# Kernel optimization log

Measured on AMD Instinct MI355X. Metric: run time of the kernel, lower is better.

## Reference

```python
import jax, jax.numpy as jnp
import numpy as np

N_NODES = 100000
N_EDGES = 1600000
NODE_F = 8   # augmented node features
EDGE_F = 2   # augmented edge features
GLOB_F = 1
HID = 16
L = 3        # message passing steps

EDGE_IN = GLOB_F + EDGE_F + 2 * NODE_F   # 19
NODE_IN = GLOB_F + EDGE_F + NODE_F       # 11
GLOB_IN = EDGE_F + NODE_F + GLOB_F       # 11


def setup_inputs() -> dict:
    key = jax.random.key(0)
    ks = jax.random.split(key, 20)
    inp = {
        "x": jax.random.normal(ks[0], (N_NODES, NODE_F), dtype=jnp.float32),
        "edge_index": jax.random.randint(ks[1], (2, N_EDGES), 0, N_NODES, dtype=jnp.int32),
        "edge_attr": jax.random.normal(ks[2], (N_EDGES, EDGE_F), dtype=jnp.float32),
        "g": jax.random.normal(ks[3], (1, GLOB_F), dtype=jnp.float32),
    }
    s = 0.1
    inp["edge_W1"] = jax.random.normal(ks[4], (L, EDGE_IN, HID), dtype=jnp.float32) * s
    inp["edge_b1"] = jnp.zeros((L, HID), dtype=jnp.float32)
    inp["edge_W2"] = jax.random.normal(ks[5], (L, HID, EDGE_F), dtype=jnp.float32) * s
    inp["edge_b2"] = jnp.zeros((L, EDGE_F), dtype=jnp.float32)
    inp["node_W1"] = jax.random.normal(ks[6], (L, NODE_IN, HID), dtype=jnp.float32) * s
    inp["node_b1"] = jnp.zeros((L, HID), dtype=jnp.float32)
    inp["node_W2"] = jax.random.normal(ks[7], (L, HID, NODE_F), dtype=jnp.float32) * s
    inp["node_b2"] = jnp.zeros((L, NODE_F), dtype=jnp.float32)
    inp["glob_W1"] = jax.random.normal(ks[8], (L, GLOB_IN, HID), dtype=jnp.float32) * s
    inp["glob_b1"] = jnp.zeros((L, HID), dtype=jnp.float32)
    inp["glob_W2"] = jax.random.normal(ks[9], (L, HID, GLOB_F), dtype=jnp.float32) * s
    inp["glob_b2"] = jnp.zeros((L, GLOB_F), dtype=jnp.float32)
    return inp


def _mlp(h, W1, b1, W2, b2):
    # two-layer MLP with ReLU after first layer only (activate_final=False, no layer_norm)
    return jnp.maximum(h @ W1 + b1, 0.0) @ W2 + b2


def reference(x, edge_index, edge_attr, g,
              edge_W1, edge_b1, edge_W2, edge_b2,
              node_W1, node_b1, node_W2, node_b2,
              glob_W1, glob_b1, glob_W2, glob_b2):
    row, col = edge_index[0], edge_index[1]
    n = x.shape[0]
    for l in range(L):
        g_e = jnp.broadcast_to(g, (row.shape[0], GLOB_F))
        # edge block: gather node features along edges, concat, MLP -> [E, EDGE_F]
        e_in = jnp.concatenate([g_e, x[row], x[col], edge_attr], axis=1)
        edge_emb = _mlp(e_in, edge_W1[l], edge_b1[l], edge_W2[l], edge_b2[l])
        # sum-aggregate edge embeddings to source nodes
        agg = jax.ops.segment_sum(edge_emb, row, num_segments=n)
        g_n = jnp.broadcast_to(g, (n, GLOB_F))
        node_emb = _mlp(jnp.concatenate([g_n, x, agg], axis=1),
                        node_W1[l], node_b1[l], node_W2[l], node_b2[l])
        # global block on mean-aggregated edge/node embeddings
        edge_gl = jnp.mean(edge_emb, axis=0, keepdims=True)
        node_gl = jnp.mean(node_emb, axis=0, keepdims=True)
        g = _mlp(jnp.concatenate([node_gl, edge_gl, g], axis=1),
                 glob_W1[l], glob_b1[l], glob_W2[l], glob_b2[l])
        x, edge_attr = node_emb, edge_emb
    return x  # final node embeddings [N, NODE_F]
```

## Files before the change

kernel.cpp:

```cpp
#include <hip/hip_runtime.h>

#define NN 100000
#define NE 1600000
#define CH 4096
#define NCHUNK ((NE + CH - 1) / CH)
#define NBUCK ((NN + 255) / 256)
#define SUB 4

__device__ __forceinline__ float wave_red(float v) {
#pragma unroll
    for (int off = 32; off > 0; off >>= 1) v += __shfl_down(v, off, 64);
    return v;
}

__global__ __launch_bounds__(256) void hist_kernel(
    const int* __restrict__ ei, int* __restrict__ hist)
{
    __shared__ int h[NBUCK];
    int t = threadIdx.x, c = blockIdx.x;
    for (int b = t; b < NBUCK; b += 256) h[b] = 0;
    __syncthreads();
    int base = c * CH;
    for (int i = t; i < CH; i += 256) {
        int e = base + i;
        if (e < NE) atomicAdd(&h[ei[e] >> 8], 1);
    }
    __syncthreads();
    for (int b = t; b < NBUCK; b += 256) hist[c * NBUCK + b] = h[b];
}

__global__ __launch_bounds__(512) void bscan_kernel(
    const int* __restrict__ hist, int* __restrict__ baseT, int* __restrict__ colTotal)
{
    __shared__ int buf[2][512];
    int b = blockIdx.x, t = threadIdx.x;
    int v = (t < NCHUNK) ? hist[t * NBUCK + b] : 0;
    buf[0][t] = v;
    __syncthreads();
    int src = 0;
    for (int d = 1; d < 512; d <<= 1) {
        int nv = buf[src][t] + ((t >= d) ? buf[src][t - d] : 0);
        buf[src ^ 1][t] = nv;
        src ^= 1;
        __syncthreads();
    }
    if (t < NCHUNK) baseT[b * NCHUNK + t] = buf[src][t] - v;
    if (t == NCHUNK - 1) colTotal[b] = buf[src][t];
}

__global__ __launch_bounds__(512) void boff_kernel(
    const int* __restrict__ colTotal, int* __restrict__ b_off)
{
    __shared__ int buf[2][512];
    int t = threadIdx.x;
    int v = (t < NBUCK) ? colTotal[t] : 0;
    buf[0][t] = v;
    __syncthreads();
    int src = 0;
    for (int d = 1; d < 512; d <<= 1) {
        int nv = buf[src][t] + ((t >= d) ? buf[src][t - d] : 0);
        buf[src ^ 1][t] = nv;
        src ^= 1;
        __syncthreads();
    }
    if (t < NBUCK) b_off[t] = buf[src][t] - v;
    if (t == NBUCK - 1) b_off[NBUCK] = buf[src][t];
}

__global__ __launch_bounds__(256) void fillb_kernel(
    const int* __restrict__ ei, const float* __restrict__ eattr,
    const int* __restrict__ baseT, const int* __restrict__ b_off,
    float4* __restrict__ rec)
{
    __shared__ int sslot[NBUCK];
    int t = threadIdx.x, c = blockIdx.x;
    for (int b = t; b < NBUCK; b += 256)
        sslot[b] = b_off[b] + baseT[b * NCHUNK + c];
    __syncthreads();
    int base = c * CH;
    for (int i = t; i < CH; i += 256) {
        int e = base + i;
        if (e < NE) {
            int row = ei[e];
            int slot = atomicAdd(&sslot[row >> 8], 1);
            float2 ea = reinterpret_cast<const float2*>(eattr)[e];
            float4 v;
            v.x = __int_as_float(row);
            v.y = __int_as_float(ei[NE + e]);
            v.z = ea.x; v.w = ea.y;
            rec[slot] = v;
        }
    }
}

template <bool WRITE_EMB, bool NEED_SUM>
__global__ __launch_bounds__(256, 1) void edge_kernel(
    float4* __restrict__ rec, const int* __restrict__ b_off,
    const float* __restrict__ gptr,
    const float* __restrict__ eW1, const float* __restrict__ eB1,
    const float* __restrict__ eW2, const float* __restrict__ eB2,
    const float* __restrict__ xin,
    float2* __restrict__ pagg, float* __restrict__ sums)
{
    __shared__ float sPr[256][20];
    __shared__ float sagg[256][2];
    __shared__ float redE[4][2];
    int tid = threadIdx.x;
    int b = blockIdx.x >> 2, s = blockIdx.x & 3;
    int n0 = b << 8;
    sagg[tid][0] = 0.f; sagg[tid][1] = 0.f;

    float gval = gptr[0];
    int nrow = n0 + tid;
    if (nrow < NN) {
        const float4* xi = reinterpret_cast<const float4*>(xin + (size_t)nrow * 8);
        float4 a0 = xi[0], a1 = xi[1];
        float xv[8] = {a0.x, a0.y, a0.z, a0.w, a1.x, a1.y, a1.z, a1.w};
        float pr[16];
#pragma unroll
        for (int q = 0; q < 16; q++) pr[q] = 0.f;
#pragma unroll
        for (int k = 0; k < 8; k++) {
            float v = xv[k];
#pragma unroll
            for (int q = 0; q < 16; q++) pr[q] += v * eW1[(1 + k) * 16 + q];
        }
        float4* pw = reinterpret_cast<float4*>(&sPr[tid][0]);
#pragma unroll
        for (int t4 = 0; t4 < 4; t4++)
            pw[t4] = make_float4(pr[4*t4], pr[4*t4+1], pr[4*t4+2], pr[4*t4+3]);
    }
    __syncthreads();

    float cw[128], aw[32], ow[32], gterm[16];
    {
        const float4* W4 = reinterpret_cast<const float4*>(eW1 + 9 * 16);
#pragma unroll
        for (int i = 0; i < 32; i++) {
            float4 w = W4[i];
            cw[4*i] = w.x; cw[4*i+1] = w.y; cw[4*i+2] = w.z; cw[4*i+3] = w.w;
        }
        const float4* A4 = reinterpret_cast<const float4*>(eW1 + 17 * 16);
#pragma unroll
        for (int i = 0; i < 8; i++) {
            float4 w = A4[i];
            aw[4*i] = w.x; aw[4*i+1] = w.y; aw[4*i+2] = w.z; aw[4*i+3] = w.w;
        }
        const float4* O4 = reinterpret_cast<const float4*>(eW2);
#pragma unroll
        for (int i = 0; i < 8; i++) {
            float4 w = O4[i];
            ow[4*i] = w.x; ow[4*i+1] = w.y; ow[4*i+2] = w.z; ow[4*i+3] = w.w;
        }
#pragma unroll
        for (int q = 0; q < 16; q++) gterm[q] = eB1[q] + gval * eW1[q];
    }
    float b20 = eB2[0], b21 = eB2[1];

    int e0b = b_off[b], e1b = b_off[b + 1];
    int qlen = (e1b - e0b + SUB - 1) / SUB;
    int es = e0b + s * qlen;
    int ee = min(e1b, es + qlen);

    float t0 = 0.f, t1 = 0.f;
    for (int e = es + tid; e < ee; e += 256) {
        float4 r = rec[e];
        int li  = __float_as_int(r.x) - n0;
        int col = __float_as_int(r.y);
        const float4* xc4 = reinterpret_cast<const float4*>(xin + (size_t)col * 8);
        float4 c0 = xc4[0], c1 = xc4[1];
        const float4* pr4 = reinterpret_cast<const float4*>(&sPr[li][0]);
        float4 p0 = pr4[0], p1 = pr4[1], p2 = pr4[2], p3 = pr4[3];
        float h[16];
        h[0]  = gterm[0]  + p0.x; h[1]  = gterm[1]  + p0.y;
        h[2]  = gterm[2]  + p0.z; h[3]  = gterm[3]  + p0.w;
        h[4]  = gterm[4]  + p1.x; h[5]  = gterm[5]  + p1.y;
        h[6]  = gterm[6]  + p1.z; h[7]  = gterm[7]  + p1.w;
        h[8]  = gterm[8]  + p2.x; h[9]  = gterm[9]  + p2.y;
        h[10] = gterm[10] + p2.z; h[11] = gterm[11] + p2.w;
        h[12] = gterm[12] + p3.x; h[13] = gterm[13] + p3.y;
        h[14] = gterm[14] + p3.z; h[15] = gterm[15] + p3.w;
        float xc[8] = {c0.x, c0.y, c0.z, c0.w, c1.x, c1.y, c1.z, c1.w};
#pragma unroll
        for (int k = 0; k < 8; k++) {
            float v = xc[k];
#pragma unroll
            for (int q = 0; q < 16; q++) h[q] += v * cw[k * 16 + q];
        }
#pragma unroll
        for (int q = 0; q < 16; q++) h[q] += r.z * aw[q] + r.w * aw[16 + q];
        float s0 = b20, s1 = b21;
#pragma unroll
        for (int q = 0; q < 16; q++) {
            float rr = fmaxf(h[q], 0.f);
            s0 += rr * ow[2 * q];
            s1 += rr * ow[2 * q + 1];
        }
        if (WRITE_EMB) rec[e] = make_float4(r.x, r.y, s0, s1);
        atomicAdd(&sagg[li][0], s0);
        atomicAdd(&sagg[li][1], s1);
        t0 += s0; t1 += s1;
    }

    if (NEED_SUM) {
        float r0 = wave_red(t0), r1 = wave_red(t1);
        int wave = tid >> 6, lane = tid & 63;
        if (lane == 0) { redE[wave][0] = r0; redE[wave][1] = r1; }
    }
    __syncthreads();
    pagg[((size_t)s * NBUCK + b) * 256 + tid] =
        make_float2(sagg[tid][0], sagg[tid][1]);
    if (NEED_SUM && tid == 0) {
        atomicAdd(&sums[0], redE[0][0] + redE[1][0] + redE[2][0] + redE[3][0]);
        atomicAdd(&sums[1], redE[0][1] + redE[1][1] + redE[2][1] + redE[3][1]);
    }
}

template <bool NEED_SUM>
__global__ __launch_bounds__(256) void node_kernel(
    const float* __restrict__ xin, const float2* __restrict__ pagg,
    const float* __restrict__ gptr,
    const float* __restrict__ nW1, const float* __restrict__ nB1,
    const float* __restrict__ nW2, const float* __restrict__ nB2,
    float* __restrict__ xout, float* __restrict__ sums)
{
    __shared__ float redN[4][8];
    int tid = threadIdx.x, b = blockIdx.x;
    int n = b * 256 + tid;
    float out[8];
#pragma unroll
    for (int m = 0; m < 8; m++) out[m] = 0.f;

    if (n < NN) {
        float ag0 = 0.f, ag1 = 0.f;
#pragma unroll
        for (int s = 0; s < SUB; s++) {
            float2 p = pagg[((size_t)s * NBUCK + b) * 256 + tid];
            ag0 += p.x; ag1 += p.y;
        }
        float gval = gptr[0];
        float in[11];
        in[0] = gval;
        const float4* xi = reinterpret_cast<const float4*>(xin + (size_t)n * 8);
        float4 a0 = xi[0], a1 = xi[1];
        in[1] = a0.x; in[2] = a0.y; in[3] = a0.z; in[4] = a0.w;
        in[5] = a1.x; in[6] = a1.y; in[7] = a1.z; in[8] = a1.w;
        in[9] = ag0; in[10] = ag1;

        float h[16];
#pragma unroll
        for (int q = 0; q < 16; q++) h[q] = nB1[q];
#pragma unroll
        for (int k = 0; k < 11; k++) {
            float v = in[k];
#pragma unroll
            for (int q = 0; q < 16; q++) h[q] += v * nW1[k * 16 + q];
        }
#pragma unroll
        for (int m = 0; m < 8; m++) out[m] = nB2[m];
#pragma unroll
        for (int q = 0; q < 16; q++) {
            float hq = fmaxf(h[q], 0.f);
#pragma unroll
            for (int m = 0; m < 8; m++) out[m] += hq * nW2[q * 8 + m];
        }
        float4* xo = reinterpret_cast<float4*>(xout + (size_t)n * 8);
        xo[0] = make_float4(out[0], out[1], out[2], out[3]);
        xo[1] = make_float4(out[4], out[5], out[6], out[7]);
    }
    if (NEED_SUM) {
        float r[8];
#pragma unroll
        for (int m = 0; m < 8; m++) r[m] = wave_red(out[m]);
        int wave = tid >> 6, lane = tid & 63;
        if (lane == 0) {
#pragma unroll
            for (int m = 0; m < 8; m++) redN[wave][m] = r[m];
        }
        __syncthreads();
        if (tid == 0) {
#pragma unroll
            for (int m = 0; m < 8; m++) {
                float s = redN[0][m] + redN[1][m] + redN[2][m] + redN[3][m];
                atomicAdd(&sums[2 + m], s);
            }
        }
    }
}

__global__ void glob_kernel(const float* __restrict__ sums,
                            const float* __restrict__ gold,
                            const float* __restrict__ W1, const float* __restrict__ B1,
                            const float* __restrict__ W2, const float* __restrict__ B2,
                            float* __restrict__ gnew)
{
    if (threadIdx.x == 0 && blockIdx.x == 0) {
        float in[11];
#pragma unroll
        for (int j = 0; j < 8; j++) in[j] = sums[2 + j] * (1.0f / NN);
        in[8] = sums[0] * (1.0f / NE);
        in[9] = sums[1] * (1.0f / NE);
        in[10] = gold[0];
        float acc = B2[0];
#pragma unroll
        for (int j = 0; j < 16; j++) {
            float h = B1[j];
#pragma unroll
            for (int k = 0; k < 11; k++) h += in[k] * W1[k * 16 + j];
            acc += fmaxf(h, 0.f) * W2[j];
        }
        gnew[0] = acc;
    }
}

extern "C" void kernel_launch(void* const* d_in, const int* in_sizes, int n_in,
                              void* d_out, int out_size, void* d_ws, size_t ws_size,
                              hipStream_t stream) {
    const float* x     = (const float*)d_in[0];
    const int*   ei    = (const int*)d_in[1];
    const float* eattr = (const float*)d_in[2];
    const float* g     = (const float*)d_in[3];
    const float* eW1 = (const float*)d_in[4];
    const float* eB1 = (const float*)d_in[5];
    const float* eW2 = (const float*)d_in[6];
    const float* eB2 = (const float*)d_in[7];
    const float* nW1 = (const float*)d_in[8];
    const float* nB1 = (const float*)d_in[9];
    const float* nW2 = (const float*)d_in[10];
    const float* nB2 = (const float*)d_in[11];
    const float* gW1 = (const float*)d_in[12];
    const float* gB1 = (const float*)d_in[13];
    const float* gW2 = (const float*)d_in[14];
    const float* gB2 = (const float*)d_in[15];
    float* out = (float*)d_out;

    char* ws = (char*)d_ws;
    float*  xb0   = (float*)(ws);
    float*  xb1   = (float*)(ws + 3200000);
    int*    b_off = (int*)  (ws + 6400000);
    float*  sums  = (float*)(ws + 6401600);
    float*  g1    = (float*)(ws + 6401728);
    float*  g2    = g1 + 1;
    float4* rec   = (float4*)(ws + 6401792);
    float2* pagg  = (float2*)(ws + 32001792);
    int*    hist     = (int*)xb1;
    int*    baseT    = (int*)((char*)xb1 + 611584);
    int*    colTotal = (int*)((char*)xb1 + 1223168);

    dim3 blk(256);
    dim3 cgrid(NCHUNK);
    dim3 bgrid(NBUCK);
    dim3 egrid(NBUCK * SUB);

    hipMemsetAsync(sums, 0, 128, stream);
    hist_kernel<<<cgrid, blk, 0, stream>>>(ei, hist);
    bscan_kernel<<<bgrid, 512, 0, stream>>>(hist, baseT, colTotal);
    boff_kernel<<<1, 512, 0, stream>>>(colTotal, b_off);
    fillb_kernel<<<cgrid, blk, 0, stream>>>(ei, eattr, baseT, b_off, rec);

    edge_kernel<true, true><<<egrid, blk, 0, stream>>>(
        rec, b_off, g, eW1, eB1, eW2, eB2, x, pagg, sums);
    node_kernel<true><<<bgrid, blk, 0, stream>>>(
        x, pagg, g, nW1, nB1, nW2, nB2, xb0, sums);
    glob_kernel<<<1, 64, 0, stream>>>(sums, g, gW1, gB1, gW2, gB2, g1);

    edge_kernel<true, true><<<egrid, blk, 0, stream>>>(
        rec, b_off, g1, eW1 + 304, eB1 + 16, eW2 + 32, eB2 + 2, xb0, pagg, sums + 16);
    node_kernel<true><<<bgrid, blk, 0, stream>>>(
        xb0, pagg, g1, nW1 + 176, nB1 + 16, nW2 + 128, nB2 + 8, xb1, sums + 16);
    glob_kernel<<<1, 64, 0, stream>>>(sums + 16, g1, gW1 + 176, gB1 + 16, gW2 + 16, gB2 + 1, g2);

    edge_kernel<false, false><<<egrid, blk, 0, stream>>>(
        rec, b_off, g2, eW1 + 608, eB1 + 32, eW2 + 64, eB2 + 4, xb1, pagg, sums);
    node_kernel<false><<<bgrid, blk, 0, stream>>>(
        xb1, pagg, g2, nW1 + 352, nB1 + 32, nW2 + 256, nB2 + 16, out, sums);
}
```

Measured before the change: 388.0 us.

## Fuse node MLP into edge kernel via last-block-done counter

The node update now runs inside the edge kernel: each of the four sub-blocks per node bucket bumps a per-bucket atomic counter, and the last one to finish reads the partial aggregates and computes the node MLP. This removes three node kernel launches and their inter-kernel gaps. It also folds the bias and global term into the per-node precompute, writes only the two embedding floats back to the record, and pins the weight arrays in registers with empty asm. The cost is threadfences, extra counter memory that must be zeroed each call, and higher register pressure in the edge kernel.

Measured after the change: 1.134 ms. +192.4%, slower.

```diff
diff --git a/kernel.cpp b/kernel.cpp
--- a/kernel.cpp
+++ b/kernel.cpp
@@ -100,11 +100,16 @@
     const float* __restrict__ eW1, const float* __restrict__ eB1,
     const float* __restrict__ eW2, const float* __restrict__ eB2,
     const float* __restrict__ xin,
-    float2* __restrict__ pagg, float* __restrict__ sums)
+    const float* __restrict__ nW1, const float* __restrict__ nB1,
+    const float* __restrict__ nW2, const float* __restrict__ nB2,
+    float2* __restrict__ pagg, int* __restrict__ cnt,
+    float* __restrict__ xout, float* __restrict__ sums)
 {
     __shared__ float sPr[256][20];
     __shared__ float sagg[256][2];
     __shared__ float redE[4][2];
+    __shared__ float redN[4][8];
+    __shared__ int   isLast;
     int tid = threadIdx.x;
     int b = blockIdx.x >> 2, s = blockIdx.x & 3;
     int n0 = b << 8;
@@ -118,7 +123,7 @@
         float xv[8] = {a0.x, a0.y, a0.z, a0.w, a1.x, a1.y, a1.z, a1.w};
         float pr[16];
 #pragma unroll
-        for (int q = 0; q < 16; q++) pr[q] = 0.f;
+        for (int q = 0; q < 16; q++) pr[q] = eB1[q] + gval * eW1[q];
 #pragma unroll
         for (int k = 0; k < 8; k++) {
             float v = xv[k];
@@ -132,7 +137,7 @@
     }
     __syncthreads();
 
-    float cw[128], aw[32], ow[32], gterm[16];
+    float cw[128], aw[32], ow[32];
     {
         const float4* W4 = reinterpret_cast<const float4*>(eW1 + 9 * 16);
 #pragma unroll
@@ -152,9 +157,13 @@
             float4 w = O4[i];
             ow[4*i] = w.x; ow[4*i+1] = w.y; ow[4*i+2] = w.z; ow[4*i+3] = w.w;
         }
-#pragma unroll
-        for (int q = 0; q < 16; q++) gterm[q] = eB1[q] + gval * eW1[q];
-    }
+    }
+#pragma unroll
+    for (int i = 0; i < 128; i++) asm volatile("" : "+v"(cw[i]));
+#pragma unroll
+    for (int i = 0; i < 32; i++)  asm volatile("" : "+v"(aw[i]));
+#pragma unroll
+    for (int i = 0; i < 32; i++)  asm volatile("" : "+v"(ow[i]));
     float b20 = eB2[0], b21 = eB2[1];
 
     int e0b = b_off[b], e1b = b_off[b + 1];
@@ -172,14 +181,10 @@
         const float4* pr4 = reinterpret_cast<const float4*>(&sPr[li][0]);
         float4 p0 = pr4[0], p1 = pr4[1], p2 = pr4[2], p3 = pr4[3];
         float h[16];
-        h[0]  = gterm[0]  + p0.x; h[1]  = gterm[1]  + p0.y;
-        h[2]  = gterm[2]  + p0.z; h[3]  = gterm[3]  + p0.w;
-        h[4]  = gterm[4]  + p1.x; h[5]  = gterm[5]  + p1.y;
-        h[6]  = gterm[6]  + p1.z; h[7]  = gterm[7]  + p1.w;
-        h[8]  = gterm[8]  + p2.x; h[9]  = gterm[9]  + p2.y;
-        h[10] = gterm[10] + p2.z; h[11] = gterm[11] + p2.w;
-        h[12] = gterm[12] + p3.x; h[13] = gterm[13] + p3.y;
-        h[14] = gterm[14] + p3.z; h[15] = gterm[15] + p3.w;
+        h[0]  = p0.x; h[1]  = p0.y; h[2]  = p0.z; h[3]  = p0.w;
+        h[4]  = p1.x; h[5]  = p1.y; h[6]  = p1.z; h[7]  = p1.w;
+        h[8]  = p2.x; h[9]  = p2.y; h[10] = p2.z; h[11] = p2.w;
+        h[12] = p3.x; h[13] = p3.y; h[14] = p3.z; h[15] = p3.w;
         float xc[8] = {c0.x, c0.y, c0.z, c0.w, c1.x, c1.y, c1.z, c1.w};
 #pragma unroll
         for (int k = 0; k < 8; k++) {
@@ -196,7 +201,8 @@
             s0 += rr * ow[2 * q];
             s1 += rr * ow[2 * q + 1];
         }
-        if (WRITE_EMB) rec[e] = make_float4(r.x, r.y, s0, s1);
+        if (WRITE_EMB)
+            reinterpret_cast<float2*>(rec)[2 * e + 1] = make_float2(s0, s1);
         atomicAdd(&sagg[li][0], s0);
         atomicAdd(&sagg[li][1], s1);
         t0 += s0; t1 += s1;
@@ -214,31 +220,23 @@
         atomicAdd(&sums[0], redE[0][0] + redE[1][0] + redE[2][0] + redE[3][0]);
         atomicAdd(&sums[1], redE[0][1] + redE[1][1] + redE[2][1] + redE[3][1]);
     }
-}
-
-template <bool NEED_SUM>
-__global__ __launch_bounds__(256) void node_kernel(
-    const float* __restrict__ xin, const float2* __restrict__ pagg,
-    const float* __restrict__ gptr,
-    const float* __restrict__ nW1, const float* __restrict__ nB1,
-    const float* __restrict__ nW2, const float* __restrict__ nB2,
-    float* __restrict__ xout, float* __restrict__ sums)
-{
-    __shared__ float redN[4][8];
-    int tid = threadIdx.x, b = blockIdx.x;
-    int n = b * 256 + tid;
+    __threadfence();
+    if (tid == 0) isLast = (atomicAdd(&cnt[b], 1) == SUB - 1);
+    __syncthreads();
+    if (!isLast) return;
+
+    __threadfence();
     float out[8];
 #pragma unroll
     for (int m = 0; m < 8; m++) out[m] = 0.f;
-
+    int n = n0 + tid;
     if (n < NN) {
         float ag0 = 0.f, ag1 = 0.f;
 #pragma unroll
-        for (int s = 0; s < SUB; s++) {
-            float2 p = pagg[((size_t)s * NBUCK + b) * 256 + tid];
+        for (int ss = 0; ss < SUB; ss++) {
+            float2 p = pagg[((size_t)ss * NBUCK + b) * 256 + tid];
             ag0 += p.x; ag1 += p.y;
         }
-        float gval = gptr[0];
         float in[11];
         in[0] = gval;
         const float4* xi = reinterpret_cast<const float4*>(xin + (size_t)n * 8);
@@ -281,8 +279,8 @@
         if (tid == 0) {
 #pragma unroll
             for (int m = 0; m < 8; m++) {
-                float s = redN[0][m] + redN[1][m] + redN[2][m] + redN[3][m];
-                atomicAdd(&sums[2 + m], s);
+                float sv = redN[0][m] + redN[1][m] + redN[2][m] + redN[3][m];
+                atomicAdd(&sums[2 + m], sv);
             }
         }
     }
@@ -339,10 +337,11 @@
     float*  xb1   = (float*)(ws + 3200000);
     int*    b_off = (int*)  (ws + 6400000);
     float*  sums  = (float*)(ws + 6401600);
-    float*  g1    = (float*)(ws + 6401728);
+    int*    cnt   = (int*)  (ws + 6401728);
+    float*  g1    = (float*)(ws + 6406528);
     float*  g2    = g1 + 1;
-    float4* rec   = (float4*)(ws + 6401792);
-    float2* pagg  = (float2*)(ws + 32001792);
+    float4* rec   = (float4*)(ws + 6406592);
+    float2* pagg  = (float2*)(ws + 32006592);
     int*    hist     = (int*)xb1;
     int*    baseT    = (int*)((char*)xb1 + 611584);
     int*    colTotal = (int*)((char*)xb1 + 1223168);
@@ -352,26 +351,23 @@
     dim3 bgrid(NBUCK);
     dim3 egrid(NBUCK * SUB);
 
-    hipMemsetAsync(sums, 0, 128, stream);
+    hipMemsetAsync(sums, 0, 4928, stream);
     hist_kernel<<<cgrid, blk, 0, stream>>>(ei, hist);
     bscan_kernel<<<bgrid, 512, 0, stream>>>(hist, baseT, colTotal);
     boff_kernel<<<1, 512, 0, stream>>>(colTotal, b_off);
     fillb_kernel<<<cgrid, blk, 0, stream>>>(ei, eattr, baseT, b_off, rec);
 
     edge_kernel<true, true><<<egrid, blk, 0, stream>>>(
-        rec, b_off, g, eW1, eB1, eW2, eB2, x, pagg, sums);
-    node_kernel<true><<<bgrid, blk, 0, stream>>>(
-        x, pagg, g, nW1, nB1, nW2, nB2, xb0, sums);
+        rec, b_off, g, eW1, eB1, eW2, eB2, x,
+        nW1, nB1, nW2, nB2, pagg, cnt, xb0, sums);
     glob_kernel<<<1, 64, 0, stream>>>(sums, g, gW1, gB1, gW2, gB2, g1);
 
     edge_kernel<true, true><<<egrid, blk, 0, stream>>>(
-        rec, b_off, g1, eW1 + 304, eB1 + 16, eW2 + 32, eB2 + 2, xb0, pagg, sums + 16);
-    node_kernel<true><<<bgrid, blk, 0, stream>>>(
-        xb0, pagg, g1, nW1 + 176, nB1 + 16, nW2 + 128, nB2 + 8, xb1, sums + 16);
+        rec, b_off, g1, eW1 + 304, eB1 + 16, eW2 + 32, eB2 + 2, xb0,
+        nW1 + 176, nB1 + 16, nW2 + 128, nB2 + 8, pagg, cnt + NBUCK, xb1, sums + 16);
     glob_kernel<<<1, 64, 0, stream>>>(sums + 16, g1, gW1 + 176, gB1 + 16, gW2 + 16, gB2 + 1, g2);
 
     edge_kernel<false, false><<<egrid, blk, 0, stream>>>(
-        rec, b_off, g2, eW1 + 608, eB1 + 32, eW2 + 64, eB2 + 4, xb1, pagg, sums);
-    node_kernel<false><<<bgrid, blk, 0, stream>>>(
-        xb1, pagg, g2, nW1 + 352, nB1 + 32, nW2 + 256, nB2 + 16, out, sums);
-}
+        rec, b_off, g2, eW1 + 608, eB1 + 32, eW2 + 64, eB2 + 4, xb1,
+        nW1 + 352, nB1 + 32, nW2 + 256, nB2 + 16, pagg, cnt + 2 * NBUCK, out, sums);
+}
```
